# Optimization experiments

Measured on AMD Instinct MI355X. Metric: run time of the kernel, lower is better.

The kernel has to match this reference:

```python
import jax, jax.numpy as jnp
import numpy as np

B, TE, H = 32, 8192, 128  # batch, encoder seq len, hidden

def setup_inputs() -> dict:
    key = jax.random.key(0)
    k1, k2, k3, k4, k5 = jax.random.split(key, 5)
    return {
        "encoder_out_seq": jax.random.normal(k1, (B, TE, H), dtype=jnp.float32),
        "decoder_out_seq": jax.random.normal(k2, (B, 1, H), dtype=jnp.float32),
        "W_a": jax.random.normal(k3, (H, H), dtype=jnp.float32) * 0.05,
        "U_a": jax.random.normal(k4, (H, H), dtype=jnp.float32) * 0.05,
        "V_a": jax.random.normal(k5, (H, 1), dtype=jnp.float32) * 0.05,
    }

def reference(encoder_out_seq, decoder_out_seq, W_a, U_a, V_a):
    # W_a . s : [B, TE, H]
    Ws = jnp.einsum('beh,hk->bek', encoder_out_seq, W_a)
    # U_a . h : [B, 1, H] (single decoder step, broadcasts over TE)
    Uh = jnp.einsum('bdh,hk->bdk', decoder_out_seq, U_a)
    # energy scores: tanh then project to scalar -> [B, TE]
    scores = jnp.einsum('bek,ko->be', jnp.tanh(Ws + Uh), V_a)
    e_i = jax.nn.softmax(scores, axis=-1)            # [B, TE]
    c_i = jnp.einsum('be,beh->bh', e_i, encoder_out_seq)  # context [B, H]
    return (e_i, c_i)
```

## Files before the change

### kernel.cpp

```cpp
#include <hip/hip_runtime.h>
#include <hip/hip_bf16.h>

#define B_  32
#define TE_ 8192
#define H_  128
#define M_  (B_ * TE_)

typedef __bf16 bf16x8 __attribute__((ext_vector_type(8)));
typedef __bf16 bf16x4 __attribute__((ext_vector_type(4)));
typedef float  f32x4  __attribute__((ext_vector_type(4)));

#define WS_UH    0
#define WS_WP    4096
#define WS_LACC  (4096 + 8192)
#define WS_CACC  (WS_LACC + 32)

#define SROW 272

__device__ __forceinline__ float tanh_fast(float x) {
  x = fminf(10.f, fmaxf(-10.f, x));
  float e = __expf(2.f * x);
  return (e - 1.f) * __builtin_amdgcn_rcpf(e + 1.f);
}

__global__ __launch_bounds__(256) void prep_kernel(
    const float* __restrict__ dec, const float* __restrict__ U,
    const float* __restrict__ W, float* __restrict__ ws) {
  __shared__ float ldsU[H_ * H_];
  __shared__ float ldsd[H_];
  int b = blockIdx.x, t = threadIdx.x;

  float4* l4 = (float4*)ldsU;
  const float4* g4 = (const float4*)U;
  #pragma unroll
  for (int i = 0; i < 16; ++i) l4[t + 256 * i] = g4[t + 256 * i];
  if (t < 32) ((float4*)ldsd)[t] = ((const float4*)(dec + b * H_))[t];
  __syncthreads();

  if (t < H_) {
    float s = 0.f;
    #pragma unroll
    for (int h = 0; h < H_; ++h) s += ldsd[h] * ldsU[h * H_ + t];
    ws[WS_UH + b * H_ + t] = s;
    ws[WS_CACC + b * H_ + t] = 0.f;
  }
  if (t == 0) ws[WS_LACC + b] = 0.f;

  if (t < 64) {
    int nt = b >> 2, sK = b & 3;
    int kk0 = sK * 32 + ((t >> 4) & 3) * 8;
    int nn = nt * 16 + (t & 15);
    __bf16* Wp = (__bf16*)(ws + WS_WP);
    #pragma unroll
    for (int j = 0; j < 8; ++j)
      Wp[(b * 64 + t) * 8 + j] = (__bf16)W[(kk0 + j) * H_ + nn];
  }
}

__global__ __launch_bounds__(256, 3) void fused_kernel(
    const float* __restrict__ enc, const float* __restrict__ ws_in,
    const float* __restrict__ V, float* __restrict__ wout,
    float* __restrict__ ws) {
  __shared__ uint4 ldsW[2048];
  __shared__ float ldsUV[256];
  __shared__ float lsum[4];
  __shared__ __align__(16) unsigned char ldsS[4][16 * SROW];

  int t = threadIdx.x, wave = t >> 6, lane = t & 63;
  int l15 = lane & 15, quad = lane >> 4;
  int blockRow = blockIdx.x << 8;
  int b = blockRow >> 13;

  const char* gbase = (const char*)enc + (size_t)(blockRow + (wave << 4)) * (H_ * 4);
  f32x4 ld[8];
  #pragma unroll
  for (int i = 0; i < 8; ++i)
    ld[i] = __builtin_nontemporal_load((const f32x4*)(gbase + i * 1024 + lane * 16));

  const uint4* wsrc = (const uint4*)(ws_in + WS_WP);
  for (int i = t; i < 2048; i += 256) ldsW[i] = wsrc[i];
  if (t < 128) ldsUV[t] = ws_in[WS_UH + b * H_ + t];
  else ldsUV[t] = V[t - 128];
  __syncthreads();

  float cacc[32];
  #pragma unroll
  for (int k = 0; k < 32; ++k) cacc[k] = 0.f;
  float Lpart = 0.f;

  unsigned char* sb = ldsS[wave];
  int wrhi = lane >> 5, wc = lane & 31;

  #pragma unroll
  for (int it = 0; it < 4; ++it) {
    uint2 hp[8];
    #pragma unroll
    for (int i = 0; i < 8; ++i) {
      union { bf16x4 h; uint2 u; } cv;
      cv.h[0] = (__bf16)ld[i][0]; cv.h[1] = (__bf16)ld[i][1];
      cv.h[2] = (__bf16)ld[i][2]; cv.h[3] = (__bf16)ld[i][3];
      hp[i] = cv.u;
    }
    if (it < 3) {
      #pragma unroll
      for (int i = 0; i < 8; ++i)
        ld[i] = __builtin_nontemporal_load(
            (const f32x4*)(gbase + (it + 1) * 32768 + i * 1024 + lane * 16));
    }
    #pragma unroll
    for (int i = 0; i < 8; ++i)
      *(uint2*)(sb + (2 * i + wrhi) * SROW + wc * 8) = hp[i];

    bf16x8 af[4];
    #pragma unroll
    for (int s = 0; s < 4; ++s)
      af[s] = *(const bf16x8*)(sb + l15 * SROW + s * 64 + quad * 16);

    float p = 0.f;
    #pragma unroll
    for (int nt = 0; nt < 8; ++nt) {
      f32x4 acc = {0.f, 0.f, 0.f, 0.f};
      #pragma unroll
      for (int s = 0; s < 4; ++s) {
        union { uint4 u; bf16x8 v; } bw;
        bw.u = ldsW[(nt * 4 + s) * 64 + lane];
        acc = __builtin_amdgcn_mfma_f32_16x16x32_bf16(bw.v, af[s], acc, 0, 0, 0);
      }
      float4 u4 = ((const float4*)ldsUV)[nt * 4 + quad];
      float4 v4 = ((const float4*)(ldsUV + 128))[nt * 4 + quad];
      p += tanh_fast(acc[0] + u4.x) * v4.x;
      p += tanh_fast(acc[1] + u4.y) * v4.y;
      p += tanh_fast(acc[2] + u4.z) * v4.z;
      p += tanh_fast(acc[3] + u4.w) * v4.w;
    }
    p += __shfl_xor(p, 16, 64);
    p += __shfl_xor(p, 32, 64);
    float w = __expf(p);

    int rowBase = blockRow + ((it * 4 + wave) << 4);
    if (quad == 0) wout[rowBase + l15] = w;
    Lpart += w;

    #pragma unroll
    for (int s = 0; s < 4; ++s)
      #pragma unroll
      for (int j = 0; j < 8; ++j)
        cacc[s * 8 + j] += w * (float)af[s][j];
  }

  #pragma unroll
  for (int m = 1; m < 16; m <<= 1) {
    #pragma unroll
    for (int k = 0; k < 32; ++k)
      cacc[k] += __shfl_xor(cacc[k], m, 64);
  }
  Lpart += __shfl_xor(Lpart, 1, 64);
  Lpart += __shfl_xor(Lpart, 2, 64);
  Lpart += __shfl_xor(Lpart, 4, 64);
  Lpart += __shfl_xor(Lpart, 8, 64);

  __syncthreads();
  float* pcbuf = (float*)ldsW;
  if (l15 == 0) {
    #pragma unroll
    for (int s = 0; s < 4; ++s)
      #pragma unroll
      for (int j = 0; j < 8; ++j)
        pcbuf[wave * H_ + s * 32 + quad * 8 + j] = cacc[s * 8 + j];
  }
  if (lane == 0) lsum[wave] = Lpart;
  __syncthreads();

  if (t < H_) {
    float s = pcbuf[0 * H_ + t] + pcbuf[1 * H_ + t] + pcbuf[2 * H_ + t] + pcbuf[3 * H_ + t];
    atomicAdd(&ws[WS_CACC + b * H_ + t], s);
  }
  if (t == 0)
    atomicAdd(&ws[WS_LACC + b], lsum[0] + lsum[1] + lsum[2] + lsum[3]);
}

__global__ __launch_bounds__(256) void finalize_kernel(
    float* __restrict__ e, float* __restrict__ c, const float* __restrict__ ws) {
  int t = threadIdx.x;
  if (blockIdx.x < 256) {
    int i4 = blockIdx.x * 256 + t;
    int b = i4 >> 11;
    float inv = 1.f / ws[WS_LACC + b];
    float4 v = ((float4*)e)[i4];
    v.x *= inv; v.y *= inv; v.z *= inv; v.w *= inv;
    ((float4*)e)[i4] = v;
  } else {
    #pragma unroll
    for (int k = 0; k < 16; ++k) {
      int i = k * 256 + t;
      int b = i >> 7;
      c[i] = ws[WS_CACC + i] / ws[WS_LACC + b];
    }
  }
}

extern "C" void kernel_launch(void* const* d_in, const int* in_sizes, int n_in,
                              void* d_out, int out_size, void* d_ws, size_t ws_size,
                              hipStream_t stream) {
  const float* enc = (const float*)d_in[0];
  const float* dec = (const float*)d_in[1];
  const float* Wa  = (const float*)d_in[2];
  const float* Ua  = (const float*)d_in[3];
  const float* Va  = (const float*)d_in[4];

  float* out   = (float*)d_out;
  float* e_out = out;
  float* c_out = out + B_ * TE_;
  float* ws    = (float*)d_ws;

  prep_kernel<<<B_, 256, 0, stream>>>(dec, Ua, Wa, ws);
  fused_kernel<<<M_ / 256, 256, 0, stream>>>(enc, ws, Va, e_out, ws);
  finalize_kernel<<<257, 256, 0, stream>>>(e_out, c_out, ws);
}
```

Before: 207.9 us.

## Fold prep kernel into fused kernel and replace atomics with per-block partials

Removes the separate prep launch: each block of the fused kernel now converts W_a to the packed bf16 MFMA layout and computes U_a·dec for its batch directly into LDS. Cross-block accumulation of softmax denominators and context vectors switches from global atomics to per-block partial buffers, which finalize reduces. This saves a launch and the atomics-zeroing dependency, but every one of 1024 blocks redundantly reads W and U (mostly from L2) and does a 128x128 matvec before starting its main work.

New measurement: 208.4 us. About the same (+0.2%).

```diff
diff --git a/kernel.cpp b/kernel.cpp
--- a/kernel.cpp
+++ b/kernel.cpp
@@ -1,5 +1,4 @@
 #include <hip/hip_runtime.h>
-#include <hip/hip_bf16.h>
 
 #define B_  32
 #define TE_ 8192
@@ -10,10 +9,8 @@
 typedef __bf16 bf16x4 __attribute__((ext_vector_type(4)));
 typedef float  f32x4  __attribute__((ext_vector_type(4)));
 
-#define WS_UH    0
-#define WS_WP    4096
-#define WS_LACC  (4096 + 8192)
-#define WS_CACC  (WS_LACC + 32)
+#define WS_PL 0
+#define WS_PC 1024
 
 #define SROW 272
 
@@ -23,42 +20,9 @@
   return (e - 1.f) * __builtin_amdgcn_rcpf(e + 1.f);
 }
 
-__global__ __launch_bounds__(256) void prep_kernel(
-    const float* __restrict__ dec, const float* __restrict__ U,
-    const float* __restrict__ W, float* __restrict__ ws) {
-  __shared__ float ldsU[H_ * H_];
-  __shared__ float ldsd[H_];
-  int b = blockIdx.x, t = threadIdx.x;
-
-  float4* l4 = (float4*)ldsU;
-  const float4* g4 = (const float4*)U;
-  #pragma unroll
-  for (int i = 0; i < 16; ++i) l4[t + 256 * i] = g4[t + 256 * i];
-  if (t < 32) ((float4*)ldsd)[t] = ((const float4*)(dec + b * H_))[t];
-  __syncthreads();
-
-  if (t < H_) {
-    float s = 0.f;
-    #pragma unroll
-    for (int h = 0; h < H_; ++h) s += ldsd[h] * ldsU[h * H_ + t];
-    ws[WS_UH + b * H_ + t] = s;
-    ws[WS_CACC + b * H_ + t] = 0.f;
-  }
-  if (t == 0) ws[WS_LACC + b] = 0.f;
-
-  if (t < 64) {
-    int nt = b >> 2, sK = b & 3;
-    int kk0 = sK * 32 + ((t >> 4) & 3) * 8;
-    int nn = nt * 16 + (t & 15);
-    __bf16* Wp = (__bf16*)(ws + WS_WP);
-    #pragma unroll
-    for (int j = 0; j < 8; ++j)
-      Wp[(b * 64 + t) * 8 + j] = (__bf16)W[(kk0 + j) * H_ + nn];
-  }
-}
-
 __global__ __launch_bounds__(256, 3) void fused_kernel(
-    const float* __restrict__ enc, const float* __restrict__ ws_in,
+    const float* __restrict__ enc, const float* __restrict__ dec,
+    const float* __restrict__ W, const float* __restrict__ U,
     const float* __restrict__ V, float* __restrict__ wout,
     float* __restrict__ ws) {
   __shared__ uint4 ldsW[2048];
@@ -77,9 +41,43 @@
   for (int i = 0; i < 8; ++i)
     ld[i] = __builtin_nontemporal_load((const f32x4*)(gbase + i * 1024 + lane * 16));
 
-  const uint4* wsrc = (const uint4*)(ws_in + WS_WP);
-  for (int i = t; i < 2048; i += 256) ldsW[i] = wsrc[i];
-  if (t < 128) ldsUV[t] = ws_in[WS_UH + b * H_ + t];
+  float* ldsP = (float*)ldsS;
+  float* ldsd = ((float*)ldsS) + 256;
+  if (t < 32) ((float4*)ldsd)[t] = ((const float4*)(dec + b * H_))[t];
+  {
+    unsigned int* w32 = (unsigned int*)ldsW;
+    int c32 = t & 31, r8 = t >> 5;
+    #pragma unroll
+    for (int p = 0; p < 8; ++p) {
+      int kA = p * 16 + r8 * 2;
+      float4 rA = ((const float4*)(W + kA * H_))[c32];
+      float4 rB = ((const float4*)(W + (kA + 1) * H_))[c32];
+      float fa[4] = {rA.x, rA.y, rA.z, rA.w};
+      float fb[4] = {rB.x, rB.y, rB.z, rB.w};
+      #pragma unroll
+      for (int c = 0; c < 4; ++c) {
+        int n = c32 * 4 + c;
+        union { __bf16 h[2]; unsigned int u; } pk;
+        pk.h[0] = (__bf16)fa[c]; pk.h[1] = (__bf16)fb[c];
+        int E = ((n >> 4) * 4 + (kA >> 5)) * 512
+              + (((kA >> 3) & 3) * 16 + (n & 15)) * 8 + (kA & 7);
+        w32[E >> 1] = pk.u;
+      }
+    }
+  }
+  __syncthreads();
+
+  {
+    int col = t & 127, half = t >> 7;
+    const float* Up = U + (half * 64) * H_ + col;
+    const float* dp = ldsd + half * 64;
+    float s = 0.f;
+    #pragma unroll
+    for (int h = 0; h < 64; ++h) s += dp[h] * Up[h * H_];
+    ldsP[t] = s;
+  }
+  __syncthreads();
+  if (t < 128) ldsUV[t] = ldsP[t] + ldsP[t + 128];
   else ldsUV[t] = V[t - 128];
   __syncthreads();
 
@@ -173,28 +171,47 @@
 
   if (t < H_) {
     float s = pcbuf[0 * H_ + t] + pcbuf[1 * H_ + t] + pcbuf[2 * H_ + t] + pcbuf[3 * H_ + t];
-    atomicAdd(&ws[WS_CACC + b * H_ + t], s);
+    ws[WS_PC + blockIdx.x * H_ + t] = s;
   }
   if (t == 0)
-    atomicAdd(&ws[WS_LACC + b], lsum[0] + lsum[1] + lsum[2] + lsum[3]);
+    ws[WS_PL + blockIdx.x] = lsum[0] + lsum[1] + lsum[2] + lsum[3];
 }
 
 __global__ __launch_bounds__(256) void finalize_kernel(
     float* __restrict__ e, float* __restrict__ c, const float* __restrict__ ws) {
   int t = threadIdx.x;
   if (blockIdx.x < 256) {
+    __shared__ float sL;
+    int b = blockIdx.x >> 3;
+    if (t == 0) {
+      float L = 0.f;
+      #pragma unroll
+      for (int k = 0; k < 32; ++k) L += ws[WS_PL + b * 32 + k];
+      sL = L;
+    }
+    __syncthreads();
+    float inv = 1.f / sL;
     int i4 = blockIdx.x * 256 + t;
-    int b = i4 >> 11;
-    float inv = 1.f / ws[WS_LACC + b];
     float4 v = ((float4*)e)[i4];
     v.x *= inv; v.y *= inv; v.z *= inv; v.w *= inv;
     ((float4*)e)[i4] = v;
   } else {
-    #pragma unroll
-    for (int k = 0; k < 16; ++k) {
-      int i = k * 256 + t;
-      int b = i >> 7;
-      c[i] = ws[WS_CACC + i] / ws[WS_LACC + b];
+    __shared__ float Ls[32];
+    if (t < 32) {
+      float L = 0.f;
+      #pragma unroll
+      for (int k = 0; k < 32; ++k) L += ws[WS_PL + t * 32 + k];
+      Ls[t] = L;
+    }
+    __syncthreads();
+    #pragma unroll
+    for (int kk = 0; kk < 16; ++kk) {
+      int i = kk * 256 + t;
+      int bb = i >> 7, h = i & 127;
+      float s = 0.f;
+      #pragma unroll
+      for (int k = 0; k < 32; ++k) s += ws[WS_PC + (bb * 32 + k) * H_ + h];
+      c[i] = s / Ls[bb];
     }
   }
 }
@@ -213,7 +230,6 @@
   float* c_out = out + B_ * TE_;
   float* ws    = (float*)d_ws;
 
-  prep_kernel<<<B_, 256, 0, stream>>>(dec, Ua, Wa, ws);
-  fused_kernel<<<M_ / 256, 256, 0, stream>>>(enc, ws, Va, e_out, ws);
+  fused_kernel<<<M_ / 256, 256, 0, stream>>>(enc, dec, Wa, Ua, Va, e_out, ws);
   finalize_kernel<<<257, 256, 0, stream>>>(e_out, c_out, ws);
 }
```
